# Kernel optimization log

Hardware: AMD Instinct MI355X
Metric: run time of the kernel (lower is better)

Reference implementation:

```python
import jax, jax.numpy as jnp
import numpy as np

DIM = 512
HEADS = 8
DIM_HEAD = 64  # scale constant from __init__; also dim // heads here
SCALE = DIM_HEAD ** -0.5


def setup_inputs() -> dict:
    key = jax.random.key(0)
    k1, k2, k3, k4 = jax.random.split(key, 4)
    x = jax.random.normal(k1, (2, 4096, DIM), dtype=jnp.float32)
    # nn.Linear weights: stored as [out, in]; we keep [in, out] for x @ W
    w_qkv = jax.random.normal(k2, (DIM, 3 * DIM), dtype=jnp.float32) * (DIM ** -0.5)
    w_out = jax.random.normal(k3, (DIM, DIM), dtype=jnp.float32) * (DIM ** -0.5)
    b_out = jax.random.normal(k4, (DIM,), dtype=jnp.float32) * 0.02
    return {"x": x, "w_qkv": w_qkv, "w_out": w_out, "b_out": b_out}


def reference(x, w_qkv, w_out, b_out):
    B, N, C = x.shape
    H = HEADS
    Dh = C // H
    qkv = x @ w_qkv                                   # [B, N, 3C]
    q, k, v = jnp.split(qkv, 3, axis=-1)
    # [B, N, C] -> [B, H, N, Dh]
    reshape = lambda t: t.reshape(B, N, H, Dh).transpose(0, 2, 1, 3)
    q, k, v = reshape(q), reshape(k), reshape(v)
    attn = jnp.einsum("bhnd,bhmd->bhnm", q, k) * SCALE  # [B, H, N, N]
    attn = jax.nn.softmax(attn, axis=-1)
    out = jnp.einsum("bhnm,bhmd->bhnd", attn, v)       # [B, H, N, Dh]
    out = out.transpose(0, 2, 1, 3).reshape(B, N, C)
    return out @ w_out + b_out
```

## Files before the change

kernel.cpp:

```cpp
#include <hip/hip_runtime.h>
#include <stdint.h>

typedef unsigned short u16;
typedef __bf16 bf16x8 __attribute__((ext_vector_type(8)));
typedef float fx4 __attribute__((ext_vector_type(4)));
typedef float fx16 __attribute__((ext_vector_type(16)));


__device__ __forceinline__ u16 f2bf(float f) {
    unsigned int u = __float_as_uint(f);
    u += 0x7fffu + ((u >> 16) & 1u);
    return (u16)(u >> 16);
}

__device__ __forceinline__ bf16x8 ld8(const u16* p) {
    return __builtin_bit_cast(bf16x8, *(const int4*)p);
}

__device__ __forceinline__ uint32_t pk2bf(float lo, float hi) {
    uint32_t a = __float_as_uint(lo) + 0x8000u;
    uint32_t b = __float_as_uint(hi) + 0x8000u;
    return __builtin_amdgcn_perm(b, a, 0x07060302u);
}

typedef __attribute__((address_space(3))) uint32_t lds_u32;
typedef __attribute__((address_space(1))) const uint32_t glb_u32;
__device__ __forceinline__ void glds16(const u16* g, u16* l) {
    __builtin_amdgcn_global_load_lds((glb_u32*)g, (lds_u32*)l, 16, 0, 0);
}


__global__ __launch_bounds__(256) void cast_x_kernel(const float* __restrict__ x,
                                                     u16* __restrict__ xb) {
    int idx = blockIdx.x * 256 + threadIdx.x;
    const float4* p = (const float4*)(x + (size_t)idx * 8);
    float4 a = p[0], b = p[1];
    int4 v;
    v.x = (int)pk2bf(a.x, a.y); v.y = (int)pk2bf(a.z, a.w);
    v.z = (int)pk2bf(b.x, b.y); v.w = (int)pk2bf(b.z, b.w);
    *(int4*)(xb + (size_t)idx * 8) = v;
}


__global__ __launch_bounds__(256) void transpose_cast_kernel(const float* __restrict__ w_qkv,
                                                             u16* __restrict__ wqkv_t,
                                                             const float* __restrict__ w_out,
                                                             u16* __restrict__ wout_t) {
    __shared__ float T[64][65];
    int t = threadIdx.x;
    int bx = blockIdx.x;
    const float* in; u16* out; int NR = 512, NC;
    if (bx < 24) { in = w_qkv; out = wqkv_t; NC = 1536; }
    else         { in = w_out; out = wout_t; NC = 512; bx -= 24; }
    int i0 = blockIdx.y * 64, j0 = bx * 64;
    int r = t >> 4, cc = t & 15;
#pragma unroll
    for (int j = 0; j < 4; ++j) {
        int row = r + j * 16;
        float4 v = *(const float4*)(in + (size_t)(i0 + row) * NC + j0 + cc * 4);
        T[row][cc * 4 + 0] = v.x; T[row][cc * 4 + 1] = v.y;
        T[row][cc * 4 + 2] = v.z; T[row][cc * 4 + 3] = v.w;
    }
    __syncthreads();
#pragma unroll
    for (int j = 0; j < 4; ++j) {
        int jr = r + j * 16;
        unsigned int u0 = f2bf(T[cc * 4 + 0][jr]) | ((unsigned int)f2bf(T[cc * 4 + 1][jr]) << 16);
        unsigned int u1 = f2bf(T[cc * 4 + 2][jr]) | ((unsigned int)f2bf(T[cc * 4 + 3][jr]) << 16);
        uint2 u; u.x = u0; u.y = u1;
        *(uint2*)(out + (size_t)(j0 + jr) * NR + i0 + cc * 4) = u;
    }
}


#define QSCALE 0.180336880f

template<int MODE>
__global__ __launch_bounds__(256) void gemm_kernel(const u16* __restrict__ A,
                                                   const u16* __restrict__ Bt,
                                                   u16* __restrict__ Qf,
                                                   u16* __restrict__ Kf,
                                                   u16* __restrict__ Vf,
                                                   const float* __restrict__ bias,
                                                   float* __restrict__ Out,
                                                   int Ncols) {
    __shared__ __align__(16) u16 Sh[16384];
    int tid = threadIdx.x;
    int w = tid >> 6, lane = tid & 63;
    int m16 = lane & 15, quad = lane >> 4;
    int ntn = Ncols / 128;
    int g = blockIdx.x;
    int xcd = g & 7, j = g >> 3;
    int by = xcd + 8 * (j / ntn);
    int bx = j % ntn;
    int r0 = by * 128, c0 = bx * 128;
    int wr = w >> 1, wc = w & 1;
    int lrow = lane >> 2, lchk = (lane & 3) * 8;

    fx4 acc[4][4] = {};

    for (int k0 = 0; k0 < 512; k0 += 32) {
        __syncthreads();
#pragma unroll
        for (int jj = 0; jj < 2; ++jj) {
            int rw = jj * 64 + w * 16;
            glds16(A  + (size_t)(r0 + rw + lrow) * 512 + k0 + lchk, &Sh[rw * 32]);
            glds16(Bt + (size_t)(c0 + rw + lrow) * 512 + k0 + lchk, &Sh[4096 + rw * 32]);
        }
        __syncthreads();
        bf16x8 af[4], bfr[4];
#pragma unroll
        for (int t = 0; t < 4; ++t) {
            af[t]  = ld8(&Sh[(wr * 64 + t * 16 + m16) * 32 + quad * 8]);
            bfr[t] = ld8(&Sh[4096 + (wc * 64 + t * 16 + m16) * 32 + quad * 8]);
        }
#pragma unroll
        for (int mt = 0; mt < 4; ++mt)
#pragma unroll
            for (int nt = 0; nt < 4; ++nt)
                acc[mt][nt] = __builtin_amdgcn_mfma_f32_16x16x32_bf16(af[mt], bfr[nt], acc[mt][nt], 0, 0, 0);
    }

    if (MODE == 0) {
        int sec = c0 >> 9;
        __syncthreads();
        if (sec <= 1) {
            float sc = (sec == 0) ? QSCALE : 1.0f;
#pragma unroll
            for (int mt = 0; mt < 4; ++mt)
#pragma unroll
                for (int nt = 0; nt < 4; ++nt) {
                    int lb = wc * 16 + (wr * 2 + (mt >> 1)) * 4 + nt;
                    int eb = lb * 512 + (m16 >> 3) * 256 + ((mt & 1) * 16 + quad * 4) * 8 + (m16 & 7);
#pragma unroll
                    for (int r = 0; r < 4; ++r)
                        Sh[eb + r * 8] = f2bf(acc[mt][nt][r] * sc);
                }
        } else {
#pragma unroll
            for (int mt = 0; mt < 4; ++mt)
#pragma unroll
                for (int nt = 0; nt < 4; ++nt) {
                    int lb = wc * 16 + wr * 8 + (nt >> 1) * 4 + mt;
                    int eb = lb * 512 + (quad & 1) * 256 + ((nt & 1) * 16 + m16) * 8 + (quad >> 1) * 4;
                    unsigned int u0 = f2bf(acc[mt][nt][0]) | ((unsigned int)f2bf(acc[mt][nt][1]) << 16);
                    unsigned int u1 = f2bf(acc[mt][nt][2]) | ((unsigned int)f2bf(acc[mt][nt][3]) << 16);
                    uint2 u; u.x = u0; u.y = u1;
                    *(uint2*)&Sh[eb] = u;
                }
        }
        __syncthreads();
        int b_ = r0 >> 12, n0 = r0 & 4095, hd0 = (c0 >> 6) & 7;
        u16* dst; size_t gb0;
        if (sec == 0)      { dst = Qf; gb0 = (size_t)(n0 >> 5) * 2048; }
        else if (sec == 1) { dst = Kf; gb0 = (size_t)(n0 >> 5) * 2048; }
        else               { dst = Vf; gb0 = (size_t)(n0 >> 6) * 4096; }
        int hl = tid >> 7;
        size_t gbase = (size_t)(b_ * 8 + hd0 + hl) * 262144 + gb0 + (size_t)(tid & 127) * 64;
#pragma unroll
        for (int s = 0; s < 8; ++s)
            *(int4*)(dst + gbase + s * 8) = *(const int4*)&Sh[tid * 64 + s * 8];
    } else {
#pragma unroll
        for (int mt = 0; mt < 4; ++mt) {
            int R0 = r0 + wr * 64 + mt * 16 + quad * 4;
#pragma unroll
            for (int nt = 0; nt < 4; ++nt) {
                int C = c0 + wc * 64 + nt * 16 + m16;
                float bv = bias[C];
#pragma unroll
                for (int r = 0; r < 4; ++r)
                    Out[(size_t)(R0 + r) * 512 + C] = acc[mt][nt][r] + bv;
            }
        }
    }
}


__device__ __forceinline__ void attn_iter(bf16x8 (&KC)[2][4], bf16x8 (&KN)[2][4],
                                          const bf16x8 (&qf)[4], const bf16x8& onesA,
                                          const fx16& Z,
                                          fx16& O0, fx16& O1, fx16& Lacc,
                                          const u16* __restrict__ Kh,
                                          const u16* __restrict__ Vh,
                                          int lane, int K0) {
    bf16x8 vf[2][4];
    {
        const u16* vb = Vh + (size_t)(K0 >> 6) * 4096 + lane * 8;
#pragma unroll
        for (int dt = 0; dt < 2; ++dt)
#pragma unroll
            for (int ch = 0; ch < 4; ++ch)
                vf[dt][ch] = ld8(vb + (dt * 4 + ch) * 512);
    }
    {
        int kn0 = (K0 + 64) & 2047;
        const u16* kb = Kh + (size_t)(kn0 >> 5) * 2048 + lane * 8;
#pragma unroll
        for (int dc = 0; dc < 4; ++dc) {
            KN[0][dc] = ld8(kb + dc * 512);
            KN[1][dc] = ld8(kb + 2048 + dc * 512);
        }
    }
    fx16 S0 = Z, S1 = Z;
#pragma unroll
    for (int dc = 0; dc < 4; ++dc) {
        S0 = __builtin_amdgcn_mfma_f32_32x32x16_bf16(KC[0][dc], qf[dc], S0, 0, 0, 0);
        S1 = __builtin_amdgcn_mfma_f32_32x32x16_bf16(KC[1][dc], qf[dc], S1, 0, 0, 0);
    }
    uint32_t pk0[8], pk1[8];
#pragma unroll
    for (int i = 0; i < 8; ++i) {
        pk0[i] = pk2bf(__builtin_amdgcn_exp2f(S0[2 * i]), __builtin_amdgcn_exp2f(S0[2 * i + 1]));
        pk1[i] = pk2bf(__builtin_amdgcn_exp2f(S1[2 * i]), __builtin_amdgcn_exp2f(S1[2 * i + 1]));
    }
#pragma unroll
    for (int c = 0; c < 4; ++c) {
        const uint32_t* pk = (c < 2) ? pk0 : pk1;
        int o = (c & 1) * 4;
        int4 bi; bi.x = (int)pk[o]; bi.y = (int)pk[o + 1]; bi.z = (int)pk[o + 2]; bi.w = (int)pk[o + 3];
        bf16x8 bfrag = __builtin_bit_cast(bf16x8, bi);
        O0 = __builtin_amdgcn_mfma_f32_32x32x16_bf16(vf[0][c], bfrag, O0, 0, 0, 0);
        O1 = __builtin_amdgcn_mfma_f32_32x32x16_bf16(vf[1][c], bfrag, O1, 0, 0, 0);
        Lacc = __builtin_amdgcn_mfma_f32_32x32x16_bf16(onesA, bfrag, Lacc, 0, 0, 0);
    }
}

__global__ __launch_bounds__(256, 2) void attn_kernel(const u16* __restrict__ Qf,
                                                      const u16* __restrict__ Kf,
                                                      const u16* __restrict__ Vf,
                                                      float* __restrict__ Part) {
    int tid = threadIdx.x;
    int w = tid >> 6, lane = tid & 63;
    int bh = ((blockIdx.x & 7) << 1) | ((blockIdx.x >> 3) & 1);
    int half = (blockIdx.x >> 4) & 1;
    int qt = blockIdx.x >> 5;

    const u16* Qh = Qf + (size_t)bh * 262144;
    const u16* Kh = Kf + (size_t)bh * 262144 + (size_t)half * 131072;
    const u16* Vh = Vf + (size_t)bh * 262144 + (size_t)half * 131072;

    bf16x8 qf[4];
    {
        const u16* qb = Qh + (size_t)(qt * 4 + w) * 2048 + lane * 8;
#pragma unroll
        for (int dc = 0; dc < 4; ++dc)
            qf[dc] = ld8(qb + dc * 512);
    }

    int4 oi; oi.x = oi.y = oi.z = oi.w = 0x3F803F80;
    const bf16x8 onesA = __builtin_bit_cast(bf16x8, oi);
    const fx16 Z = {};
    fx16 O0 = {}, O1 = {}, Lacc = {};

    bf16x8 kA[2][4], kB[2][4];
    {
        const u16* kb = Kh + lane * 8;
#pragma unroll
        for (int dc = 0; dc < 4; ++dc) {
            kA[0][dc] = ld8(kb + dc * 512);
            kA[1][dc] = ld8(kb + 2048 + dc * 512);
        }
    }

    for (int k0 = 0; k0 < 2048; k0 += 128) {
        attn_iter(kA, kB, qf, onesA, Z, O0, O1, Lacc, Kh, Vh, lane, k0);
        attn_iter(kB, kA, qf, onesA, Z, O0, O1, Lacc, Kh, Vh, lane, k0 + 64);
    }

    float* dst = Part + (size_t)(blockIdx.x * 4 + w) * 33 * 64 + lane;
#pragma unroll
    for (int r = 0; r < 16; ++r) {
        dst[r * 64]        = O0[r];
        dst[(16 + r) * 64] = O1[r];
    }
    dst[32 * 64] = Lacc[0];
}


__global__ __launch_bounds__(256) void combine_kernel(const float* __restrict__ Part,
                                                      u16* __restrict__ Ob) {
    __shared__ __align__(16) u16 Eo[4 * 32 * 68];
    int tid = threadIdx.x;
    int w = tid >> 6, lane = tid & 63;
    int q32 = lane & 31, h = lane >> 5;
    int bhcode = blockIdx.x & 15, qt = blockIdx.x >> 4;
    int bh = ((bhcode & 7) << 1) | (bhcode >> 3);
    int q0 = qt * 128;
    int p0 = (qt << 5) | bhcode, p1 = p0 | 16;

    const float* s0 = Part + (size_t)(p0 * 4 + w) * 33 * 64 + lane;
    const float* s1 = Part + (size_t)(p1 * 4 + w) * 33 * 64 + lane;
    float O0[16], O1[16];
#pragma unroll
    for (int r = 0; r < 16; ++r) {
        O0[r] = s0[r * 64] + s1[r * 64];
        O1[r] = s0[(16 + r) * 64] + s1[(16 + r) * 64];
    }
    float inv = 1.0f / (s0[32 * 64] + s1[32 * 64]);

    int ebase = w * 2176 + q32 * 68;
#pragma unroll
    for (int i = 0; i < 8; ++i) {
        int dbase = 8 * (i >> 1) + (i & 1) * 2 + 4 * h;
        uint32_t v0 = pk2bf(O0[2 * i] * inv, O0[2 * i + 1] * inv);
        uint32_t v1 = pk2bf(O1[2 * i] * inv, O1[2 * i + 1] * inv);
        *(uint32_t*)&Eo[ebase + dbase]      = v0;
        *(uint32_t*)&Eo[ebase + dbase + 32] = v1;
    }
    __syncthreads();
    int row = lane >> 1, halfc = lane & 1;
    int rb = w * 2176 + row * 68 + halfc * 32;
    int b = bh >> 3, hh = bh & 7;
    size_t gb = ((size_t)(b * 4096 + q0 + w * 32 + row)) * 512 + hh * 64 + halfc * 32;
#pragma unroll
    for (int s = 0; s < 4; ++s) {
        uint2 a = *(const uint2*)&Eo[rb + s * 8];
        uint2 c = *(const uint2*)&Eo[rb + s * 8 + 4];
        int4 v; v.x = (int)a.x; v.y = (int)a.y; v.z = (int)c.x; v.w = (int)c.y;
        *(int4*)(Ob + gb + s * 8) = v;
    }
}


extern "C" void kernel_launch(void* const* d_in, const int* in_sizes, int n_in,
                              void* d_out, int out_size, void* d_ws, size_t ws_size,
                              hipStream_t stream) {
    const float* x     = (const float*)d_in[0];
    const float* w_qkv = (const float*)d_in[1];
    const float* w_out = (const float*)d_in[2];
    const float* b_out = (const float*)d_in[3];
    float* out = (float*)d_out;

    char* ws = (char*)d_ws;
    float* Part  = (float*)(ws);
    u16* x_b     = (u16*)(ws);
    u16* wqkv_t  = (u16*)(ws + 8388608);
    u16* Qfb     = (u16*)(ws + 34603008);
    u16* Kfb     = (u16*)(ws + 42991616);
    u16* Vfb     = (u16*)(ws + 51380224);
    u16* Ob      = (u16*)(ws + 59768832);
    u16* wout_t  = (u16*)(ws + 68157440);

    cast_x_kernel<<<2048, 256, 0, stream>>>(x, x_b);
    transpose_cast_kernel<<<dim3(32, 8), 256, 0, stream>>>(w_qkv, wqkv_t, w_out, wout_t);
    gemm_kernel<0><<<768, 256, 0, stream>>>(x_b, wqkv_t, Qfb, Kfb, Vfb, nullptr, nullptr, 1536);
    attn_kernel<<<1024, 256, 0, stream>>>(Qfb, Kfb, Vfb, Part);
    combine_kernel<<<512, 256, 0, stream>>>(Part, Ob);
    gemm_kernel<1><<<256, 256, 0, stream>>>(Ob, wout_t, nullptr, nullptr, nullptr, b_out, out, 512);
}
```

Baseline: 229.8 us.

## Shrink attention key step to 32, sum softmax denominators in VALU, halve blocks

The attention kernel now processes 32 keys per step instead of 64, halving the per-step K/V fragment registers and score tile. The row-sum denominator moves from an extra MFMA against a ones matrix to a scalar VALU accumulation plus one cross-lane shuffle. Blocks shrink from 4 to 2 waves with launch bounds of 3 blocks per CU and twice the grid. The combine kernel shrinks to match and swaps __syncthreads for an lgkmcnt wait, since each wave reads back only its own LDS region. The aim is higher occupancy and fewer MFMA issues, at the cost of a longer serial loop and less K reuse across waves.

Measured after the change: 217.6 us. -5.3%, faster.

```diff
diff --git a/kernel.cpp b/kernel.cpp
--- a/kernel.cpp
+++ b/kernel.cpp
@@ -177,56 +177,53 @@
 }
 
 
-__device__ __forceinline__ void attn_iter(bf16x8 (&KC)[2][4], bf16x8 (&KN)[2][4],
-                                          const bf16x8 (&qf)[4], const bf16x8& onesA,
-                                          const fx16& Z,
-                                          fx16& O0, fx16& O1, fx16& Lacc,
-                                          const u16* __restrict__ Kh,
-                                          const u16* __restrict__ Vh,
-                                          int lane, int K0) {
-    bf16x8 vf[2][4];
+__device__ __forceinline__ void attn_iter32(bf16x8 (&KC)[4], bf16x8 (&KN)[4],
+                                            const bf16x8 (&qf)[4],
+                                            fx16& O0, fx16& O1, float& l_c,
+                                            const u16* __restrict__ Kh,
+                                            const u16* __restrict__ Vh,
+                                            int lane, int K0) {
+    bf16x8 vf[2][2];
     {
-        const u16* vb = Vh + (size_t)(K0 >> 6) * 4096 + lane * 8;
+        const u16* vb = Vh + (size_t)(K0 >> 6) * 4096 + ((K0 >> 4) & 2) * 512 + lane * 8;
 #pragma unroll
         for (int dt = 0; dt < 2; ++dt)
 #pragma unroll
-            for (int ch = 0; ch < 4; ++ch)
+            for (int ch = 0; ch < 2; ++ch)
                 vf[dt][ch] = ld8(vb + (dt * 4 + ch) * 512);
     }
     {
-        int kn0 = (K0 + 64) & 2047;
-        const u16* kb = Kh + (size_t)(kn0 >> 5) * 2048 + lane * 8;
-#pragma unroll
-        for (int dc = 0; dc < 4; ++dc) {
-            KN[0][dc] = ld8(kb + dc * 512);
-            KN[1][dc] = ld8(kb + 2048 + dc * 512);
-        }
-    }
-    fx16 S0 = Z, S1 = Z;
-#pragma unroll
-    for (int dc = 0; dc < 4; ++dc) {
-        S0 = __builtin_amdgcn_mfma_f32_32x32x16_bf16(KC[0][dc], qf[dc], S0, 0, 0, 0);
-        S1 = __builtin_amdgcn_mfma_f32_32x32x16_bf16(KC[1][dc], qf[dc], S1, 0, 0, 0);
-    }
-    uint32_t pk0[8], pk1[8];
+        int kn = (K0 + 32) & 2047;
+        const u16* kb = Kh + (size_t)(kn >> 5) * 2048 + lane * 8;
+#pragma unroll
+        for (int dc = 0; dc < 4; ++dc)
+            KN[dc] = ld8(kb + dc * 512);
+    }
+    fx16 S = {};
+#pragma unroll
+    for (int dc = 0; dc < 4; ++dc)
+        S = __builtin_amdgcn_mfma_f32_32x32x16_bf16(KC[dc], qf[dc], S, 0, 0, 0);
+    float ps = 0.0f;
+    uint32_t pk[8];
 #pragma unroll
     for (int i = 0; i < 8; ++i) {
-        pk0[i] = pk2bf(__builtin_amdgcn_exp2f(S0[2 * i]), __builtin_amdgcn_exp2f(S0[2 * i + 1]));
-        pk1[i] = pk2bf(__builtin_amdgcn_exp2f(S1[2 * i]), __builtin_amdgcn_exp2f(S1[2 * i + 1]));
-    }
-#pragma unroll
-    for (int c = 0; c < 4; ++c) {
-        const uint32_t* pk = (c < 2) ? pk0 : pk1;
-        int o = (c & 1) * 4;
-        int4 bi; bi.x = (int)pk[o]; bi.y = (int)pk[o + 1]; bi.z = (int)pk[o + 2]; bi.w = (int)pk[o + 3];
+        float a0 = __builtin_amdgcn_exp2f(S[2 * i]);
+        float a1 = __builtin_amdgcn_exp2f(S[2 * i + 1]);
+        ps += a0 + a1;
+        pk[i] = pk2bf(a0, a1);
+    }
+    l_c += ps;
+#pragma unroll
+    for (int c = 0; c < 2; ++c) {
+        int4 bi; bi.x = (int)pk[c * 4]; bi.y = (int)pk[c * 4 + 1];
+        bi.z = (int)pk[c * 4 + 2]; bi.w = (int)pk[c * 4 + 3];
         bf16x8 bfrag = __builtin_bit_cast(bf16x8, bi);
         O0 = __builtin_amdgcn_mfma_f32_32x32x16_bf16(vf[0][c], bfrag, O0, 0, 0, 0);
         O1 = __builtin_amdgcn_mfma_f32_32x32x16_bf16(vf[1][c], bfrag, O1, 0, 0, 0);
-        Lacc = __builtin_amdgcn_mfma_f32_32x32x16_bf16(onesA, bfrag, Lacc, 0, 0, 0);
-    }
-}
-
-__global__ __launch_bounds__(256, 2) void attn_kernel(const u16* __restrict__ Qf,
+    }
+}
+
+__global__ __launch_bounds__(128, 3) void attn_kernel(const u16* __restrict__ Qf,
                                                       const u16* __restrict__ Kf,
                                                       const u16* __restrict__ Vf,
                                                       float* __restrict__ Part) {
@@ -242,55 +239,54 @@
 
     bf16x8 qf[4];
     {
-        const u16* qb = Qh + (size_t)(qt * 4 + w) * 2048 + lane * 8;
+        const u16* qb = Qh + (size_t)(qt * 2 + w) * 2048 + lane * 8;
 #pragma unroll
         for (int dc = 0; dc < 4; ++dc)
             qf[dc] = ld8(qb + dc * 512);
     }
 
-    int4 oi; oi.x = oi.y = oi.z = oi.w = 0x3F803F80;
-    const bf16x8 onesA = __builtin_bit_cast(bf16x8, oi);
-    const fx16 Z = {};
-    fx16 O0 = {}, O1 = {}, Lacc = {};
-
-    bf16x8 kA[2][4], kB[2][4];
+    fx16 O0 = {}, O1 = {};
+    float l_c = 0.0f;
+
+    bf16x8 kA[4], kB[4];
     {
         const u16* kb = Kh + lane * 8;
 #pragma unroll
-        for (int dc = 0; dc < 4; ++dc) {
-            kA[0][dc] = ld8(kb + dc * 512);
-            kA[1][dc] = ld8(kb + 2048 + dc * 512);
-        }
-    }
-
-    for (int k0 = 0; k0 < 2048; k0 += 128) {
-        attn_iter(kA, kB, qf, onesA, Z, O0, O1, Lacc, Kh, Vh, lane, k0);
-        attn_iter(kB, kA, qf, onesA, Z, O0, O1, Lacc, Kh, Vh, lane, k0 + 64);
-    }
-
-    float* dst = Part + (size_t)(blockIdx.x * 4 + w) * 33 * 64 + lane;
+        for (int dc = 0; dc < 4; ++dc)
+            kA[dc] = ld8(kb + dc * 512);
+    }
+
+    for (int k0 = 0; k0 < 2048; k0 += 64) {
+        attn_iter32(kA, kB, qf, O0, O1, l_c, Kh, Vh, lane, k0);
+        attn_iter32(kB, kA, qf, O0, O1, l_c, Kh, Vh, lane, k0 + 32);
+    }
+
+    l_c += __shfl_xor(l_c, 32);
+
+    float* dst = Part + (size_t)(blockIdx.x * 2 + w) * 2112 + lane;
 #pragma unroll
     for (int r = 0; r < 16; ++r) {
         dst[r * 64]        = O0[r];
         dst[(16 + r) * 64] = O1[r];
     }
-    dst[32 * 64] = Lacc[0];
-}
-
-
-__global__ __launch_bounds__(256) void combine_kernel(const float* __restrict__ Part,
+    dst[32 * 64] = l_c;
+}
+
+
+__global__ __launch_bounds__(128) void combine_kernel(const float* __restrict__ Part,
                                                       u16* __restrict__ Ob) {
-    __shared__ __align__(16) u16 Eo[4 * 32 * 68];
+    __shared__ __align__(16) u16 Eo[2 * 32 * 68];
     int tid = threadIdx.x;
     int w = tid >> 6, lane = tid & 63;
     int q32 = lane & 31, h = lane >> 5;
     int bhcode = blockIdx.x & 15, qt = blockIdx.x >> 4;
     int bh = ((bhcode & 7) << 1) | (bhcode >> 3);
-    int q0 = qt * 128;
-    int p0 = (qt << 5) | bhcode, p1 = p0 | 16;
-
-    const float* s0 = Part + (size_t)(p0 * 4 + w) * 33 * 64 + lane;
-    const float* s1 = Part + (size_t)(p1 * 4 + w) * 33 * 64 + lane;
+    int q0 = qt * 64;
+    int p0 = ((qt << 5) | bhcode) * 2 + w;
+    int p1 = ((qt << 5) | 16 | bhcode) * 2 + w;
+
+    const float* s0 = Part + (size_t)p0 * 2112 + lane;
+    const float* s1 = Part + (size_t)p1 * 2112 + lane;
     float O0[16], O1[16];
 #pragma unroll
     for (int r = 0; r < 16; ++r) {
@@ -308,7 +304,7 @@
         *(uint32_t*)&Eo[ebase + dbase]      = v0;
         *(uint32_t*)&Eo[ebase + dbase + 32] = v1;
     }
-    __syncthreads();
+    asm volatile("s_waitcnt lgkmcnt(0)" ::: "memory");
     int row = lane >> 1, halfc = lane & 1;
     int rb = w * 2176 + row * 68 + halfc * 32;
     int b = bh >> 3, hh = bh & 7;
@@ -345,7 +341,7 @@
     cast_x_kernel<<<2048, 256, 0, stream>>>(x, x_b);
     transpose_cast_kernel<<<dim3(32, 8), 256, 0, stream>>>(w_qkv, wqkv_t, w_out, wout_t);
     gemm_kernel<0><<<768, 256, 0, stream>>>(x_b, wqkv_t, Qfb, Kfb, Vfb, nullptr, nullptr, 1536);
-    attn_kernel<<<1024, 256, 0, stream>>>(Qfb, Kfb, Vfb, Part);
-    combine_kernel<<<512, 256, 0, stream>>>(Part, Ob);
+    attn_kernel<<<2048, 128, 0, stream>>>(Qfb, Kfb, Vfb, Part);
+    combine_kernel<<<1024, 128, 0, stream>>>(Part, Ob);
     gemm_kernel<1><<<256, 256, 0, stream>>>(Ob, wout_t, nullptr, nullptr, nullptr, b_out, out, 512);
 }
```
